# Kernel optimization log

Hardware: AMD Instinct MI355X
Metric: run time of the kernel (lower is better)

## Reference

```python
import jax, jax.numpy as jnp
import numpy as np
from jax import lax

GAMMA = 2        # unused in forward (kept for fidelity to source)
PW = 10.0
THRESHOLD = 1.0
ERODE = 3
BACKZERO = 0

B, C, D, H, W = 2, 1, 128, 256, 256


def setup_inputs() -> dict:
    key = jax.random.key(0)
    k1, k2 = jax.random.split(key)
    inp = jax.random.normal(k1, (B, C, D, H, W), dtype=jnp.float32)
    tgt = jax.random.uniform(k2, (B, C, D, H, W), dtype=jnp.float32)
    return {"input": inp, "target": tgt}


def _box_sum_3d(x, r):
    # All-ones (2r+1)^3 conv3d with padding=r == sliding-window sum (shape-preserving).
    k = 2 * r + 1
    return lax.reduce_window(
        x, 0.0, lax.add,
        window_dimensions=(1, 1, k, k, k),
        window_strides=(1, 1, 1, 1, 1),
        padding=[(0, 0), (0, 0), (r, r), (r, r), (r, r)],
    )


def reference(input, target):
    # weight = clamp(target, 0, threshold); zero out voxels exactly at threshold
    w = jnp.clip(target, 0.0, THRESHOLD)
    w = w - THRESHOLD * (w == THRESHOLD).astype(jnp.float32)
    # box-filter "erosion" then binarize
    w = _box_sum_3d(w, ERODE)
    w = (w > 0).astype(jnp.float32)
    w = 1.0 + w * PW
    if BACKZERO != 0:
        mask = (input < 0).astype(jnp.float32) * (target == 0).astype(jnp.float32)
        w = w * (1.0 - mask)
    loss = jnp.abs(target - input) * w
    return jnp.mean(loss)
```

## Files before the change

### kernel.cpp

```cpp
#include <hip/hip_runtime.h>
#include <stdint.h>

#define BB 2
#define DD 128
#define HH 256
#define WW 256
static constexpr int64_t N = (int64_t)BB * DD * HH * WW;
static constexpr int WPR    = WW / 64;
static constexpr int NWORDS = BB * DD * HH * WPR;
static constexpr int ZSTR   = HH * WPR;
static constexpr int RBLOCKS = 4096;

__global__ __launch_bounds__(256) void mask_xdil(const float* __restrict__ tgt,
                                                 uint64_t* __restrict__ mask) {
    const int tid = threadIdx.x;
    const int64_t base = (int64_t)blockIdx.x * 1024;
    float4 t = ((const float4*)(tgt + base))[tid];

    unsigned nib = 0;
    nib |= (t.x > 0.0f && t.x < 1.0f) ? 1u : 0u;
    nib |= (t.y > 0.0f && t.y < 1.0f) ? 2u : 0u;
    nib |= (t.z > 0.0f && t.z < 1.0f) ? 4u : 0u;
    nib |= (t.w > 0.0f && t.w < 1.0f) ? 8u : 0u;

    __shared__ unsigned char nibs[256];
    __shared__ uint64_t words[16];
    nibs[tid] = (unsigned char)nib;
    __syncthreads();

    if (tid < 16) {
        uint64_t w = 0;
        #pragma unroll
        for (int i = 0; i < 16; i++)
            w |= (uint64_t)(nibs[tid * 16 + i] & 0xF) << (4 * i);
        words[tid] = w;
    }
    __syncthreads();

    if (tid < 16) {
        const int wx = tid & 3;
        const uint64_t C = words[tid];
        const uint64_t L = (wx > 0) ? words[tid - 1] : 0ull;
        const uint64_t R = (wx < 3) ? words[tid + 1] : 0ull;
        uint64_t d = C;
        #pragma unroll
        for (int s = 1; s <= 3; s++) {
            d |= (C << s) | (C >> s);
            d |= (L >> (64 - s));
            d |= (R << (64 - s));
        }
        mask[(int64_t)blockIdx.x * 16 + tid] = d;
    }
}

__global__ __launch_bounds__(256) void y_dil(const uint64_t* __restrict__ in,
                                             uint64_t* __restrict__ out) {
    const int n = blockIdx.x * 256 + threadIdx.x;
    const int y = (n >> 2) & (HH - 1);
    uint64_t acc = 0;
    #pragma unroll
    for (int dy = -3; dy <= 3; dy++) {
        const int yy = y + dy;
        acc |= (yy >= 0 && yy < HH) ? in[n + dy * WPR] : 0ull;
    }
    out[n] = acc;
}

__global__ __launch_bounds__(256) void z_dil(const uint64_t* __restrict__ in,
                                             uint64_t* __restrict__ out) {
    const int n = blockIdx.x * 256 + threadIdx.x;
    const int z = (n >> 10) & (DD - 1);
    uint64_t acc = 0;
    #pragma unroll
    for (int dz = -3; dz <= 3; dz++) {
        const int zz = z + dz;
        acc |= (zz >= 0 && zz < DD) ? in[n + dz * ZSTR] : 0ull;
    }
    out[n] = acc;
}

__global__ __launch_bounds__(256) void reduce_loss(const float* __restrict__ inp,
                                                   const float* __restrict__ tgt,
                                                   const uint64_t* __restrict__ mask,
                                                   double* __restrict__ partials) {
    const int64_t nvec = N / 4;
    const int64_t stride = (int64_t)RBLOCKS * 256;
    float local = 0.0f;
    for (int64_t i = (int64_t)blockIdx.x * 256 + threadIdx.x; i < nvec; i += stride) {
        float4 a = ((const float4*)inp)[i];
        float4 t = ((const float4*)tgt)[i];
        uint64_t w = mask[i >> 4];
        unsigned nib = (unsigned)(w >> ((i & 15) * 4)) & 0xFu;
        float s;
        s  = fabsf(t.x - a.x) * ((nib & 1u) ? 11.0f : 1.0f);
        s += fabsf(t.y - a.y) * ((nib & 2u) ? 11.0f : 1.0f);
        s += fabsf(t.z - a.z) * ((nib & 4u) ? 11.0f : 1.0f);
        s += fabsf(t.w - a.w) * ((nib & 8u) ? 11.0f : 1.0f);
        local += s;
    }
    #pragma unroll
    for (int off = 32; off > 0; off >>= 1)
        local += __shfl_down(local, off, 64);
    __shared__ float wsum[4];
    const int lane = threadIdx.x & 63;
    const int wv   = threadIdx.x >> 6;
    if (lane == 0) wsum[wv] = local;
    __syncthreads();
    if (threadIdx.x == 0)
        partials[blockIdx.x] = (double)(wsum[0] + wsum[1] + wsum[2] + wsum[3]);
}

__global__ __launch_bounds__(1024) void finalize(const double* __restrict__ partials,
                                                 float* __restrict__ out) {
    double local = 0.0;
    for (int i = threadIdx.x; i < RBLOCKS; i += 1024) local += partials[i];
    #pragma unroll
    for (int off = 32; off > 0; off >>= 1)
        local += __shfl_down(local, off, 64);
    __shared__ double ws[16];
    const int lane = threadIdx.x & 63;
    const int wv   = threadIdx.x >> 6;
    if (lane == 0) ws[wv] = local;
    __syncthreads();
    if (threadIdx.x == 0) {
        double s = 0.0;
        #pragma unroll
        for (int k = 0; k < 16; k++) s += ws[k];
        out[0] = (float)(s / (double)N);
    }
}

extern "C" void kernel_launch(void* const* d_in, const int* in_sizes, int n_in,
                              void* d_out, int out_size, void* d_ws, size_t ws_size,
                              hipStream_t stream) {
    const float* inp = (const float*)d_in[0];
    const float* tgt = (const float*)d_in[1];
    float* out = (float*)d_out;

    double*   partials = (double*)d_ws;
    uint64_t* mask0 = (uint64_t*)((char*)d_ws + 64 * 1024);
    uint64_t* mask1 = mask0 + NWORDS;

    mask_xdil<<<(int)(N / 1024), 256, 0, stream>>>(tgt, mask0);
    y_dil<<<NWORDS / 256, 256, 0, stream>>>(mask0, mask1);
    z_dil<<<NWORDS / 256, 256, 0, stream>>>(mask1, mask0);
    reduce_loss<<<RBLOCKS, 256, 0, stream>>>(inp, tgt, mask0, partials);
    finalize<<<1, 1024, 0, stream>>>(partials, out);
}
```

Baseline: 151.6 us.

## Fuse y/z mask dilation into one tiled LDS kernel, shuffle-based x dilation

Replaces the separate y and z dilation kernels with one kernel that loads a 16x16 (plus halo) tile of mask words into shared memory and does the separable y then z OR-dilation there. This removes one launch and one full pass over the bitmask. The x-dilation kernel now works one row per wave, using lane shuffles in place of shared memory and block syncs. The cost is halo reloads per tile and scattered 8-byte loads in the new yz kernel, which uses strided word access across wx.

```diff
diff --git a/kernel.cpp b/kernel.cpp
--- a/kernel.cpp
+++ b/kernel.cpp
@@ -8,75 +8,83 @@
 static constexpr int64_t N = (int64_t)BB * DD * HH * WW;
 static constexpr int WPR    = WW / 64;
 static constexpr int NWORDS = BB * DD * HH * WPR;
-static constexpr int ZSTR   = HH * WPR;
 static constexpr int RBLOCKS = 4096;
+
+__device__ __forceinline__ uint64_t shfl_xor_u64(uint64_t v, int lanemask) {
+    int lo = __shfl_xor((int)(uint32_t)v, lanemask, 64);
+    int hi = __shfl_xor((int)(v >> 32), lanemask, 64);
+    return ((uint64_t)(uint32_t)hi << 32) | (uint32_t)lo;
+}
 
 __global__ __launch_bounds__(256) void mask_xdil(const float* __restrict__ tgt,
                                                  uint64_t* __restrict__ mask) {
-    const int tid = threadIdx.x;
-    const int64_t base = (int64_t)blockIdx.x * 1024;
-    float4 t = ((const float4*)(tgt + base))[tid];
+    const int wave = threadIdx.x >> 6;
+    const int lane = threadIdx.x & 63;
+    const int row  = blockIdx.x * 4 + wave;
 
+    float4 t = ((const float4*)(tgt + (int64_t)row * WW))[lane];
     unsigned nib = 0;
     nib |= (t.x > 0.0f && t.x < 1.0f) ? 1u : 0u;
     nib |= (t.y > 0.0f && t.y < 1.0f) ? 2u : 0u;
     nib |= (t.z > 0.0f && t.z < 1.0f) ? 4u : 0u;
     nib |= (t.w > 0.0f && t.w < 1.0f) ? 8u : 0u;
 
-    __shared__ unsigned char nibs[256];
-    __shared__ uint64_t words[16];
-    nibs[tid] = (unsigned char)nib;
-    __syncthreads();
+    unsigned L = (unsigned)__shfl_up((int)nib, 1, 64);
+    unsigned R = (unsigned)__shfl_down((int)nib, 1, 64);
+    if (lane == 0)  L = 0;
+    if (lane == 63) R = 0;
 
-    if (tid < 16) {
-        uint64_t w = 0;
-        #pragma unroll
-        for (int i = 0; i < 16; i++)
-            w |= (uint64_t)(nibs[tid * 16 + i] & 0xF) << (4 * i);
-        words[tid] = w;
+    const unsigned m = L | (nib << 4) | (R << 8);
+    unsigned dil = 0;
+    #pragma unroll
+    for (int j = 0; j < 4; j++)
+        dil |= ((m & (0x7Fu << (j + 1))) ? 1u : 0u) << j;
+
+    uint64_t x = dil;
+    #pragma unroll
+    for (int s = 0; s < 4; s++) {
+        const int sh = 4 << s;
+        uint64_t p = shfl_xor_u64(x, 1 << s);
+        x = (lane & (1 << s)) ? (p | (x << sh)) : (x | (p << sh));
+    }
+    if ((lane & 15) == 0)
+        mask[(int64_t)row * WPR + (lane >> 4)] = x;
+}
+
+__global__ __launch_bounds__(256) void yz_dil(const uint64_t* __restrict__ in,
+                                              uint64_t* __restrict__ out) {
+    __shared__ uint64_t raw[22][23];
+    __shared__ uint64_t yd[22][17];
+    const int ty = threadIdx.x & 15;
+    const int tz = threadIdx.x >> 4;
+    const int y0 = blockIdx.x * 16;
+    const int z0 = blockIdx.y * 16;
+    const int b  = blockIdx.z >> 2;
+    const int wx = blockIdx.z & 3;
+
+    for (int idx = threadIdx.x; idx < 22 * 22; idx += 256) {
+        const int zz = idx / 22, yy = idx % 22;
+        const int gz = z0 - 3 + zz, gy = y0 - 3 + yy;
+        uint64_t v = 0;
+        if (gz >= 0 && gz < DD && gy >= 0 && gy < HH)
+            v = in[(((int64_t)(b * DD + gz)) * HH + gy) * WPR + wx];
+        raw[zz][yy] = v;
     }
     __syncthreads();
 
-    if (tid < 16) {
-        const int wx = tid & 3;
-        const uint64_t C = words[tid];
-        const uint64_t L = (wx > 0) ? words[tid - 1] : 0ull;
-        const uint64_t R = (wx < 3) ? words[tid + 1] : 0ull;
-        uint64_t d = C;
+    for (int idx = threadIdx.x; idx < 22 * 16; idx += 256) {
+        const int zz = idx >> 4, yy = idx & 15;
+        uint64_t v = 0;
         #pragma unroll
-        for (int s = 1; s <= 3; s++) {
-            d |= (C << s) | (C >> s);
-            d |= (L >> (64 - s));
-            d |= (R << (64 - s));
-        }
-        mask[(int64_t)blockIdx.x * 16 + tid] = d;
+        for (int d = 0; d < 7; d++) v |= raw[zz][yy + d];
+        yd[zz][yy] = v;
     }
-}
+    __syncthreads();
 
-__global__ __launch_bounds__(256) void y_dil(const uint64_t* __restrict__ in,
-                                             uint64_t* __restrict__ out) {
-    const int n = blockIdx.x * 256 + threadIdx.x;
-    const int y = (n >> 2) & (HH - 1);
-    uint64_t acc = 0;
+    uint64_t v = 0;
     #pragma unroll
-    for (int dy = -3; dy <= 3; dy++) {
-        const int yy = y + dy;
-        acc |= (yy >= 0 && yy < HH) ? in[n + dy * WPR] : 0ull;
-    }
-    out[n] = acc;
-}
-
-__global__ __launch_bounds__(256) void z_dil(const uint64_t* __restrict__ in,
-                                             uint64_t* __restrict__ out) {
-    const int n = blockIdx.x * 256 + threadIdx.x;
-    const int z = (n >> 10) & (DD - 1);
-    uint64_t acc = 0;
-    #pragma unroll
-    for (int dz = -3; dz <= 3; dz++) {
-        const int zz = z + dz;
-        acc |= (zz >= 0 && zz < DD) ? in[n + dz * ZSTR] : 0ull;
-    }
-    out[n] = acc;
+    for (int d = 0; d < 7; d++) v |= yd[tz + d][ty];
+    out[(((int64_t)(b * DD + z0 + tz)) * HH + y0 + ty) * WPR + wx] = v;
 }
 
 __global__ __launch_bounds__(256) void reduce_loss(const float* __restrict__ inp,
@@ -141,9 +149,8 @@
     uint64_t* mask0 = (uint64_t*)((char*)d_ws + 64 * 1024);
     uint64_t* mask1 = mask0 + NWORDS;
 
-    mask_xdil<<<(int)(N / 1024), 256, 0, stream>>>(tgt, mask0);
-    y_dil<<<NWORDS / 256, 256, 0, stream>>>(mask0, mask1);
-    z_dil<<<NWORDS / 256, 256, 0, stream>>>(mask1, mask0);
-    reduce_loss<<<RBLOCKS, 256, 0, stream>>>(inp, tgt, mask0, partials);
+    mask_xdil<<<NWORDS / 16, 256, 0, stream>>>(tgt, mask0);
+    yz_dil<<<dim3(HH / 16, DD / 16, BB * WPR), 256, 0, stream>>>(mask0, mask1);
+    reduce_loss<<<RBLOCKS, 256, 0, stream>>>(inp, tgt, mask1, partials);
     finalize<<<1, 1024, 0, stream>>>(partials, out);
 }
```

Result: no change. 151.5 us (-0.1%).
